# Kernel optimization log

Hardware: AMD Instinct MI355X
Metric: run time of the kernel (lower is better)

The kernel has to match this reference:

```python
import jax, jax.numpy as jnp
import numpy as np

B, S, H, K = 64, 512, 1024, 7

def setup_inputs() -> dict:
    key = jax.random.key(0)
    ks = jax.random.split(key, 7)
    x = jax.random.normal(ks[0], (B, S, H), dtype=jnp.float32)
    gt = jax.random.randint(ks[1], (B, S), 0, K, dtype=jnp.int64)
    mask = jnp.ones((B, S), dtype=bool)
    # learned parameters
    W = jax.random.normal(ks[2], (H, K), dtype=jnp.float32) * (1.0 / np.sqrt(H))
    b = jnp.zeros((K,), dtype=jnp.float32)
    start_trans = jax.random.uniform(ks[3], (K,), minval=-0.1, maxval=0.1)
    end_trans = jax.random.uniform(ks[4], (K,), minval=-0.1, maxval=0.1)
    trans = jax.random.uniform(ks[5], (K, K), minval=-0.1, maxval=0.1)
    return {"x": x, "gt": gt, "mask": mask, "W": W, "b": b,
            "start_trans": start_trans, "end_trans": end_trans, "trans": trans}

def _crf_neg_llh(emissions, gt, mask, start_trans, end_trans, trans):
    # emissions: [B,S,K], gt: [B,S] int, mask: [B,S] bool
    maskf = mask.astype(emissions.dtype)
    # ---- numerator: score of gold path ----
    em_at_tag = jnp.take_along_axis(emissions, gt[..., None], axis=-1)[..., 0]  # [B,S]
    trans_sc = trans[gt[:, :-1], gt[:, 1:]]                                      # [B,S-1]
    num = start_trans[gt[:, 0]] + em_at_tag[:, 0]
    num = num + jnp.sum((trans_sc + em_at_tag[:, 1:]) * maskf[:, 1:], axis=1)
    last_idx = jnp.sum(mask, axis=1).astype(jnp.int32) - 1                       # [B]
    last_tags = jnp.take_along_axis(gt, last_idx[:, None], axis=1)[:, 0]
    num = num + end_trans[last_tags]
    # ---- denominator: log partition via forward algorithm (lax.scan) ----
    alpha0 = start_trans[None, :] + emissions[:, 0]                              # [B,K]
    em_rest = jnp.transpose(emissions[:, 1:], (1, 0, 2))                         # [S-1,B,K]
    m_rest = jnp.transpose(mask[:, 1:], (1, 0))                                  # [S-1,B]
    def step(alpha, inp):
        em_t, m_t = inp
        nxt = jax.nn.logsumexp(alpha[:, :, None] + trans[None, :, :] + em_t[:, None, :], axis=1)
        return jnp.where(m_t[:, None], nxt, alpha), None
    alpha, _ = jax.lax.scan(step, alpha0, (em_rest, m_rest))
    denom = jax.nn.logsumexp(alpha + end_trans[None, :], axis=1)                 # [B]
    llh = num - denom
    return -jnp.mean(llh)  # reduction='mean', module returns negative

def reference(x, gt, mask, W, b, start_trans, end_trans, trans):
    emissions = jnp.einsum('bsh,hk->bsk', x, W) + b
    return _crf_neg_llh(emissions, gt, mask, start_trans, end_trans, trans)
```

## Files before the change

### kernel.cpp

```cpp
#include <hip/hip_runtime.h>
#include <math.h>

#define NB 64
#define NS 512
#define NH 1024
#define NK 7
#define NCHUNK 16
#define CLEN 32

#define WS_CNT     0
#define WS_ALPHA0  80
#define WS_NUMP    (WS_ALPHA0 + 64 * 8)
#define WS_CHUNKP  (WS_NUMP + 64 * 16)
#define WS_LLH     (WS_CHUNKP + 64 * 16 * 49)

typedef float f32x4 __attribute__((ext_vector_type(4)));

template <int CTRL>
__device__ __forceinline__ float dpp_add(float v) {
    const int sh = __builtin_amdgcn_update_dpp(0, __float_as_int(v),
                                               CTRL, 0xF, 0xF, true);
    return v + __int_as_float(sh);
}
template <int PAT>
__device__ __forceinline__ float swz_add(float v) {
    const int sh = __builtin_amdgcn_ds_swizzle(__float_as_int(v), PAT);
    return v + __int_as_float(sh);
}

__global__ __launch_bounds__(512)
__attribute__((amdgpu_waves_per_eu(2, 4)))
void crf_mega(
    const float* __restrict__ x, const float* __restrict__ W,
    const float* __restrict__ bias, const float* __restrict__ trans,
    const float* __restrict__ start_trans, const float* __restrict__ end_trans,
    const int* __restrict__ gt32,
    int* __restrict__ cnt, float* __restrict__ ws, float* __restrict__ out)
{
    __shared__ float lds_q[CLEN][4][9];
    __shared__ float lds_em[CLEN * 8];
    __shared__ float lds_tr[49];
    __shared__ float lds_C[NCHUNK * 49];

    float* __restrict__ alpha0g = ws + WS_ALPHA0;
    float* __restrict__ numP    = ws + WS_NUMP;
    float* __restrict__ chunkP  = ws + WS_CHUNKP;
    float* __restrict__ llh     = ws + WS_LLH;

    const int tid  = threadIdx.x;
    const int lane = tid & 63;
    const int wave = tid >> 6;
    const int q    = wave & 3;
    const int g    = wave >> 2;
    const int b = blockIdx.x >> 4;
    const int c = blockIdx.x & (NCHUNK - 1);
    const int t0 = c * CLEN;
    const int row0 = b * NS + t0;

    if (tid < 49) lds_tr[tid] = trans[tid];

    f32x4 wf0, wf1, wf2, wf3, wf4, wf5, wf6;
    {
        const float* wbase = W + (size_t)28 * (q * 64 + lane);
        asm volatile("global_load_dwordx4 %0, %1, off"            : "=v"(wf0) : "v"(wbase));
        asm volatile("global_load_dwordx4 %0, %1, off offset:16"  : "=v"(wf1) : "v"(wbase));
        asm volatile("global_load_dwordx4 %0, %1, off offset:32"  : "=v"(wf2) : "v"(wbase));
        asm volatile("global_load_dwordx4 %0, %1, off offset:48"  : "=v"(wf3) : "v"(wbase));
        asm volatile("global_load_dwordx4 %0, %1, off offset:64"  : "=v"(wf4) : "v"(wbase));
        asm volatile("global_load_dwordx4 %0, %1, off offset:80"  : "=v"(wf5) : "v"(wbase));
        asm volatile("global_load_dwordx4 %0, %1, off offset:96"  : "=v"(wf6) : "v"(wbase));
        asm volatile("s_waitcnt vmcnt(0)"
                     : "+v"(wf0), "+v"(wf1), "+v"(wf2), "+v"(wf3),
                       "+v"(wf4), "+v"(wf5), "+v"(wf6));
    }
    float wlin[28];
#pragma unroll
    for (int e = 0; e < 4; ++e) {
        wlin[e]      = wf0[e]; wlin[4 + e]  = wf1[e]; wlin[8 + e]  = wf2[e];
        wlin[12 + e] = wf3[e]; wlin[16 + e] = wf4[e]; wlin[20 + e] = wf5[e];
        wlin[24 + e] = wf6[e];
    }
#define WV(i, k) wlin[(i) * 7 + (k)]

    const float4* xq = (const float4*)(x + (size_t)row0 * NH) + q * 64 + lane;
#define PF 4
    float4 xb[PF];
#pragma unroll
    for (int j = 0; j < PF; ++j)
        xb[j] = xq[(size_t)(g + 2 * j) * (NH / 4)];

#pragma unroll
    for (int j = 0; j < 16; ++j) {
        const float4 v = xb[j & (PF - 1)];
        if (j + PF < 16)
            xb[j & (PF - 1)] = xq[(size_t)(g + 2 * (j + PF)) * (NH / 4)];
        float acc[NK];
#pragma unroll
        for (int k = 0; k < NK; ++k)
            acc[k] = v.x * WV(0, k) + v.y * WV(1, k)
                   + v.z * WV(2, k) + v.w * WV(3, k);
#pragma unroll
        for (int k = 0; k < NK; ++k) {
            acc[k] = dpp_add<0xB1>(acc[k]);
            acc[k] = dpp_add<0x4E>(acc[k]);
            acc[k] = dpp_add<0x141>(acc[k]);
        }
        const int ss = lane & 7;
        const float v01 = (ss & 1) ? acc[1] : acc[0];
        const float v23 = (ss & 1) ? acc[3] : acc[2];
        const float v45 = (ss & 1) ? acc[5] : acc[4];
        const float w03 = (ss & 2) ? v23 : v01;
        const float w47 = (ss & 2) ? acc[6] : v45;
        float r8 = (ss & 4) ? w47 : w03;
        r8 = swz_add<0x201F>(r8);
        r8 = swz_add<0x401F>(r8);
        r8 += __shfl_xor(r8, 32, 64);
        if (lane < NK) lds_q[g + 2 * j][q][lane] = r8;
    }
#undef PF
#undef WV
    __syncthreads();

    if (tid < CLEN * NK) {
        const int r = tid / NK;
        const int k = tid - r * NK;
        lds_em[r * 8 + k] = lds_q[r][0][k] + lds_q[r][1][k]
                          + lds_q[r][2][k] + lds_q[r][3][k] + bias[k];
    }
    __syncthreads();
    if (wave != 0) return;


    int oddbits = 0;
    for (int i = lane; i < 256; i += 64) oddbits |= gt32[2 * i + 1];
    const bool is64 = (__ballot(oddbits != 0) == 0ull);

    {
        const int tloc = lane & 31;
        const int tg = t0 + tloc;
        const int gidx = b * NS + tg;
        const int g2 = is64 ? gt32[2 * gidx] : gt32[gidx];
        float term = 0.f;
        if (lane < 32) {
            if (tg == 0) {
                term = start_trans[g2] + lds_em[g2];
            } else {
                const int pidx = gidx - 1;
                const int gp = is64 ? gt32[2 * pidx] : gt32[pidx];
                term = lds_tr[gp * 7 + g2] + lds_em[tloc * 8 + g2];
            }
            if (tg == NS - 1) term += end_trans[g2];
        }
#pragma unroll
        for (int m = 1; m < 64; m <<= 1) term += __shfl_xor(term, m, 64);
        if (lane == 0) numP[b * NCHUNK + c] = term;
    }

    if (c == 0 && lane < NK)
        alpha0g[b * 8 + lane] = start_trans[lane] + lds_em[lane];

    {
        const int li = lane < 49 ? lane : 48;
        const int i = li / 7;
        const int k = li - i * 7;
        float tj[NK];
#pragma unroll
        for (int j = 0; j < NK; ++j) tj[j] = lds_tr[j * 7 + k];

        const int first = (c == 0) ? 1 : 0;
        float P = lds_tr[i * 7 + k] + lds_em[first * 8 + k];
        for (int t = first + 1; t < CLEN; ++t) {
            float a[NK];
#pragma unroll
            for (int j = 0; j < NK; ++j)
                a[j] = __shfl(P, i * 7 + j, 64) + tj[j];
            const float m = fmaxf(fmaxf(fmaxf(a[0], a[1]), fmaxf(a[2], a[3])),
                                  fmaxf(fmaxf(a[4], a[5]), a[6]));
            const float su = __expf(a[0]-m) + __expf(a[1]-m) + __expf(a[2]-m)
                           + __expf(a[3]-m) + __expf(a[4]-m) + __expf(a[5]-m)
                           + __expf(a[6]-m);
            P = m + __logf(su) + lds_em[t * 8 + k];
        }
        if (lane < 49)
            chunkP[(size_t)(b * NCHUNK + c) * 49 + lane] = P;
    }

    __threadfence();
    int old = 0;
    if (lane == 0) old = atomicAdd(&cnt[b], 1);
    old = __shfl(old, 0, 64);
    if (old != NCHUNK - 1) return;
    __threadfence();

    for (int idx = lane; idx < NCHUNK * 49; idx += 64)
        lds_C[idx] = chunkP[(size_t)b * NCHUNK * 49 + idx];

    float np = (lane < NCHUNK) ? numP[b * NCHUNK + lane] : 0.f;
#pragma unroll
    for (int m = 1; m < 16; m <<= 1) np += __shfl_xor(np, m, 64);
    const float num = __shfl(np, 0, 64);

    const int kk = lane < NK ? lane : NK - 1;
    float alpha = alpha0g[b * 8 + kk];
#pragma unroll
    for (int cc = 0; cc < NCHUNK; ++cc) {
        float a[NK];
#pragma unroll
        for (int j = 0; j < NK; ++j)
            a[j] = __shfl(alpha, j, 64) + lds_C[cc * 49 + j * 7 + kk];
        const float m = fmaxf(fmaxf(fmaxf(a[0], a[1]), fmaxf(a[2], a[3])),
                              fmaxf(fmaxf(a[4], a[5]), a[6]));
        const float su = __expf(a[0]-m) + __expf(a[1]-m) + __expf(a[2]-m)
                       + __expf(a[3]-m) + __expf(a[4]-m) + __expf(a[5]-m)
                       + __expf(a[6]-m);
        alpha = m + __logf(su);
    }

    float v = (lane < NK) ? (alpha + end_trans[kk]) : -3.0e38f;
    float mv = v;
#pragma unroll
    for (int m = 1; m < 8; m <<= 1) mv = fmaxf(mv, __shfl_xor(mv, m, 64));
    float e = (lane < NK) ? __expf(v - mv) : 0.f;
#pragma unroll
    for (int m = 1; m < 8; m <<= 1) e += __shfl_xor(e, m, 64);
    if (lane == 0) llh[b] = (mv + __logf(e)) - num;

    __threadfence();
    int old2 = 0;
    if (lane == 0) old2 = atomicAdd(&cnt[NB], 1);
    old2 = __shfl(old2, 0, 64);
    if (old2 != NB - 1) return;
    __threadfence();

    float s = llh[lane];
#pragma unroll
    for (int m = 1; m < 64; m <<= 1) s += __shfl_xor(s, m, 64);
    if (lane == 0) out[0] = s * (1.0f / NB);
}

extern "C" void kernel_launch(void* const* d_in, const int* in_sizes, int n_in,
                              void* d_out, int out_size, void* d_ws, size_t ws_size,
                              hipStream_t stream)
{
    const float* x    = (const float*)d_in[0];
    const int*   gt   = (const int*)d_in[1];
    const float* W    = (const float*)d_in[3];
    const float* bias = (const float*)d_in[4];
    const float* st   = (const float*)d_in[5];
    const float* et   = (const float*)d_in[6];
    const float* tr   = (const float*)d_in[7];

    int*   cnt = (int*)d_ws;
    float* ws  = (float*)d_ws;

    (void)hipMemsetAsync(cnt, 0, 80 * sizeof(int), stream);
    crf_mega<<<NB * NCHUNK, 512, 0, stream>>>(x, W, bias, tr, st, et, gt,
                                              cnt, ws, (float*)d_out);
}
```

Before: 265.8 us.

## Split fused CRF kernel into emission/chunk kernel and separate combine kernel

Replaces the single-launch design, which used atomic counters and threadfences to elect a last block per batch and a last block overall, with two launches. The first kernel computes emissions, writes them to a workspace, and produces per-chunk transfer matrices. A second 64-block kernel computes the gold-path score, chains the chunks, and accumulates the mean into the output with atomicAdd. This removes inter-block synchronization and the waves_per_eu hint, at the cost of an extra launch plus emission writes and reads through global memory, and the float atomic order makes the result nondeterministic.

```diff
diff --git a/kernel.cpp b/kernel.cpp
--- a/kernel.cpp
+++ b/kernel.cpp
@@ -8,12 +8,6 @@
 #define NCHUNK 16
 #define CLEN 32
 
-#define WS_CNT     0
-#define WS_ALPHA0  80
-#define WS_NUMP    (WS_ALPHA0 + 64 * 8)
-#define WS_CHUNKP  (WS_NUMP + 64 * 16)
-#define WS_LLH     (WS_CHUNKP + 64 * 16 * 49)
-
 typedef float f32x4 __attribute__((ext_vector_type(4)));
 
 template <int CTRL>
@@ -28,24 +22,14 @@
     return v + __int_as_float(sh);
 }
 
-__global__ __launch_bounds__(512)
-__attribute__((amdgpu_waves_per_eu(2, 4)))
-void crf_mega(
+__global__ __launch_bounds__(512) void fused_emis_chunk(
     const float* __restrict__ x, const float* __restrict__ W,
     const float* __restrict__ bias, const float* __restrict__ trans,
-    const float* __restrict__ start_trans, const float* __restrict__ end_trans,
-    const int* __restrict__ gt32,
-    int* __restrict__ cnt, float* __restrict__ ws, float* __restrict__ out)
+    float* __restrict__ em, float* __restrict__ chunkP)
 {
     __shared__ float lds_q[CLEN][4][9];
     __shared__ float lds_em[CLEN * 8];
     __shared__ float lds_tr[49];
-    __shared__ float lds_C[NCHUNK * 49];
-
-    float* __restrict__ alpha0g = ws + WS_ALPHA0;
-    float* __restrict__ numP    = ws + WS_NUMP;
-    float* __restrict__ chunkP  = ws + WS_CHUNKP;
-    float* __restrict__ llh     = ws + WS_LLH;
 
     const int tid  = threadIdx.x;
     const int lane = tid & 63;
@@ -124,90 +108,85 @@
     if (tid < CLEN * NK) {
         const int r = tid / NK;
         const int k = tid - r * NK;
-        lds_em[r * 8 + k] = lds_q[r][0][k] + lds_q[r][1][k]
-                          + lds_q[r][2][k] + lds_q[r][3][k] + bias[k];
+        const float e = lds_q[r][0][k] + lds_q[r][1][k]
+                      + lds_q[r][2][k] + lds_q[r][3][k] + bias[k];
+        lds_em[r * 8 + k] = e;
+        em[(size_t)row0 * NK + tid] = e;
     }
     __syncthreads();
     if (wave != 0) return;
 
+    const int li = lane < 49 ? lane : 48;
+    const int i = li / 7;
+    const int k = li - i * 7;
+    float tj[NK];
+#pragma unroll
+    for (int j = 0; j < NK; ++j) tj[j] = lds_tr[j * 7 + k];
+
+    const int first = (c == 0) ? 1 : 0;
+    float P = lds_tr[i * 7 + k] + lds_em[first * 8 + k];
+    for (int t = first + 1; t < CLEN; ++t) {
+        float a[NK];
+#pragma unroll
+        for (int j = 0; j < NK; ++j)
+            a[j] = __shfl(P, i * 7 + j, 64) + tj[j];
+        const float m = fmaxf(fmaxf(fmaxf(a[0], a[1]), fmaxf(a[2], a[3])),
+                              fmaxf(fmaxf(a[4], a[5]), a[6]));
+        const float su = __expf(a[0]-m) + __expf(a[1]-m) + __expf(a[2]-m)
+                       + __expf(a[3]-m) + __expf(a[4]-m) + __expf(a[5]-m)
+                       + __expf(a[6]-m);
+        P = m + __logf(su) + lds_em[t * 8 + k];
+    }
+    if (lane < 49)
+        chunkP[(size_t)(b * NCHUNK + c) * 49 + lane] = P;
+}
+
+__global__ __launch_bounds__(64) void combine_kernel(
+    const float* __restrict__ em, const float* __restrict__ chunkP,
+    const int* __restrict__ gt32,
+    const float* __restrict__ start_trans, const float* __restrict__ end_trans,
+    const float* __restrict__ trans, float* __restrict__ out)
+{
+    __shared__ float lds_C[NCHUNK * 49];
+    __shared__ float lds_tr[49];
+    __shared__ int   lds_gt[NS];
+    const int b    = blockIdx.x;
+    const int lane = threadIdx.x;
 
     int oddbits = 0;
     for (int i = lane; i < 256; i += 64) oddbits |= gt32[2 * i + 1];
     const bool is64 = (__ballot(oddbits != 0) == 0ull);
 
-    {
-        const int tloc = lane & 31;
-        const int tg = t0 + tloc;
-        const int gidx = b * NS + tg;
-        const int g2 = is64 ? gt32[2 * gidx] : gt32[gidx];
-        float term = 0.f;
-        if (lane < 32) {
-            if (tg == 0) {
-                term = start_trans[g2] + lds_em[g2];
-            } else {
-                const int pidx = gidx - 1;
-                const int gp = is64 ? gt32[2 * pidx] : gt32[pidx];
-                term = lds_tr[gp * 7 + g2] + lds_em[tloc * 8 + g2];
-            }
-            if (tg == NS - 1) term += end_trans[g2];
-        }
-#pragma unroll
-        for (int m = 1; m < 64; m <<= 1) term += __shfl_xor(term, m, 64);
-        if (lane == 0) numP[b * NCHUNK + c] = term;
-    }
-
-    if (c == 0 && lane < NK)
-        alpha0g[b * 8 + lane] = start_trans[lane] + lds_em[lane];
-
-    {
-        const int li = lane < 49 ? lane : 48;
-        const int i = li / 7;
-        const int k = li - i * 7;
-        float tj[NK];
-#pragma unroll
-        for (int j = 0; j < NK; ++j) tj[j] = lds_tr[j * 7 + k];
-
-        const int first = (c == 0) ? 1 : 0;
-        float P = lds_tr[i * 7 + k] + lds_em[first * 8 + k];
-        for (int t = first + 1; t < CLEN; ++t) {
-            float a[NK];
-#pragma unroll
-            for (int j = 0; j < NK; ++j)
-                a[j] = __shfl(P, i * 7 + j, 64) + tj[j];
-            const float m = fmaxf(fmaxf(fmaxf(a[0], a[1]), fmaxf(a[2], a[3])),
-                                  fmaxf(fmaxf(a[4], a[5]), a[6]));
-            const float su = __expf(a[0]-m) + __expf(a[1]-m) + __expf(a[2]-m)
-                           + __expf(a[3]-m) + __expf(a[4]-m) + __expf(a[5]-m)
-                           + __expf(a[6]-m);
-            P = m + __logf(su) + lds_em[t * 8 + k];
-        }
-        if (lane < 49)
-            chunkP[(size_t)(b * NCHUNK + c) * 49 + lane] = P;
-    }
-
-    __threadfence();
-    int old = 0;
-    if (lane == 0) old = atomicAdd(&cnt[b], 1);
-    old = __shfl(old, 0, 64);
-    if (old != NCHUNK - 1) return;
-    __threadfence();
-
     for (int idx = lane; idx < NCHUNK * 49; idx += 64)
         lds_C[idx] = chunkP[(size_t)b * NCHUNK * 49 + idx];
-
-    float np = (lane < NCHUNK) ? numP[b * NCHUNK + lane] : 0.f;
-#pragma unroll
-    for (int m = 1; m < 16; m <<= 1) np += __shfl_xor(np, m, 64);
-    const float num = __shfl(np, 0, 64);
+    for (int i = lane; i < NS; i += 64) {
+        const int gidx = b * NS + i;
+        lds_gt[i] = is64 ? gt32[2 * gidx] : gt32[gidx];
+    }
+    if (lane < 49) lds_tr[lane] = trans[lane];
+    __syncthreads();
+
+    const float* emb = em + (size_t)b * NS * NK;
+    float numpart = 0.f;
+#pragma unroll
+    for (int ii = 0; ii < NS / 64; ++ii) {
+        const int t = lane + 64 * ii;
+        const int g = lds_gt[t];
+        if (t == 0) numpart += start_trans[g] + emb[g];
+        else        numpart += lds_tr[lds_gt[t - 1] * 7 + g] + emb[t * NK + g];
+    }
+#pragma unroll
+    for (int m = 1; m < 64; m <<= 1) numpart += __shfl_xor(numpart, m, 64);
+    const float num = numpart + end_trans[lds_gt[NS - 1]];
 
     const int kk = lane < NK ? lane : NK - 1;
-    float alpha = alpha0g[b * 8 + kk];
-#pragma unroll
-    for (int cc = 0; cc < NCHUNK; ++cc) {
+    float alpha = start_trans[kk] + emb[kk];
+#pragma unroll
+    for (int c = 0; c < NCHUNK; ++c) {
         float a[NK];
 #pragma unroll
         for (int j = 0; j < NK; ++j)
-            a[j] = __shfl(alpha, j, 64) + lds_C[cc * 49 + j * 7 + kk];
+            a[j] = __shfl(alpha, j, 64) + lds_C[c * 49 + j * 7 + kk];
         const float m = fmaxf(fmaxf(fmaxf(a[0], a[1]), fmaxf(a[2], a[3])),
                               fmaxf(fmaxf(a[4], a[5]), a[6]));
         const float su = __expf(a[0]-m) + __expf(a[1]-m) + __expf(a[2]-m)
@@ -223,19 +202,8 @@
     float e = (lane < NK) ? __expf(v - mv) : 0.f;
 #pragma unroll
     for (int m = 1; m < 8; m <<= 1) e += __shfl_xor(e, m, 64);
-    if (lane == 0) llh[b] = (mv + __logf(e)) - num;
-
-    __threadfence();
-    int old2 = 0;
-    if (lane == 0) old2 = atomicAdd(&cnt[NB], 1);
-    old2 = __shfl(old2, 0, 64);
-    if (old2 != NB - 1) return;
-    __threadfence();
-
-    float s = llh[lane];
-#pragma unroll
-    for (int m = 1; m < 64; m <<= 1) s += __shfl_xor(s, m, 64);
-    if (lane == 0) out[0] = s * (1.0f / NB);
+    if (lane == 0)
+        atomicAdd(out, ((mv + __logf(e)) - num) * (1.0f / NB));
 }
 
 extern "C" void kernel_launch(void* const* d_in, const int* in_sizes, int n_in,
@@ -250,10 +218,10 @@
     const float* et   = (const float*)d_in[6];
     const float* tr   = (const float*)d_in[7];
 
-    int*   cnt = (int*)d_ws;
-    float* ws  = (float*)d_ws;
-
-    (void)hipMemsetAsync(cnt, 0, 80 * sizeof(int), stream);
-    crf_mega<<<NB * NCHUNK, 512, 0, stream>>>(x, W, bias, tr, st, et, gt,
-                                              cnt, ws, (float*)d_out);
-}
+    float* em     = (float*)d_ws;
+    float* chunkP = em + (size_t)NB * NS * NK;
+
+    (void)hipMemsetAsync(d_out, 0, sizeof(float) * out_size, stream);
+    fused_emis_chunk<<<NB * NCHUNK, 512, 0, stream>>>(x, W, bias, tr, em, chunkP);
+    combine_kernel<<<NB, 64, 0, stream>>>(em, chunkP, gt, st, et, tr, (float*)d_out);
+}
```

Measured after the change: 226.2 us. 14.9% less time.
